# Optimization experiments

Measured on AMD Instinct MI355X. Metric: run time of the kernel, lower is better.

The kernel has to match this reference:

```python
import jax, jax.numpy as jnp
import numpy as np

# FP8 E4M3 constants (per FP8Handler)
E4M3_MAX = 240.0          # max_normal
MANTISSA_SCALE = 8.0      # 2 ** mantissa_bits (3)
SCALE_EPS = 1e-10


def setup_inputs() -> dict:
    key = jax.random.key(0)
    k1, k2, k3 = jax.random.split(key, 3)
    B, S, D_IN, D_OUT = 4, 2048, 4096, 4096
    x = jax.random.normal(k1, (B, S, D_IN), dtype=jnp.float32)
    weight = jax.random.normal(k2, (D_OUT, D_IN), dtype=jnp.float32)
    bias = jax.random.normal(k3, (D_OUT,), dtype=jnp.float32)
    return {"x": x, "weight": weight, "bias": bias}


def _fp8_e4m3_quant_dequant(w, scale):
    # FP8Handler.quantize_tensor + _simulate_e4m3_precision
    s = jnp.clip(w / scale, -E4M3_MAX, E4M3_MAX)
    s = s.astype(jnp.float16).astype(jnp.float32)  # fp16 round-trip
    q = jnp.round(s * MANTISSA_SCALE) / MANTISSA_SCALE  # mantissa truncation
    q = jnp.clip(q, -E4M3_MAX, E4M3_MAX)
    return q * scale


def reference(x, weight, bias):
    # FP8Quantizer.compute_scale: per-tensor max-abs, margin=0, fresh history
    amax = jnp.max(jnp.abs(weight))
    scale = jnp.maximum(amax / E4M3_MAX, SCALE_EPS)
    qw = _fp8_e4m3_quant_dequant(weight, scale)  # [out, in]
    # F.linear(x, qw, bias): x [b, s, in] @ qw.T [in, out] + bias
    return jnp.einsum('bsi,oi->bso', x, qw) + bias
```

## Files before the change

### kernel.cpp

```cpp
#include <hip/hip_runtime.h>
#include <hip/hip_bf16.h>
#include <hip/hip_fp16.h>

#define E4M3_MAX 240.0f

typedef __attribute__((ext_vector_type(8))) __bf16 bf16x8;
typedef __attribute__((ext_vector_type(4))) float f32x4;
typedef unsigned short ushort_t;

__device__ __forceinline__ void gload_lds16(const void* g, void* l) {
  __builtin_amdgcn_global_load_lds(
      (const __attribute__((address_space(1))) void*)g,
      (__attribute__((address_space(3))) void*)l,
      16, 0, 0);
}

__global__ void amax_abs_kernel(const float* __restrict__ w, int n4,
                                unsigned* __restrict__ amax_bits) {
  float m = 0.0f;
  const float4* w4 = (const float4*)w;
  int stride = gridDim.x * blockDim.x;
  for (int i = blockIdx.x * blockDim.x + threadIdx.x; i < n4; i += stride) {
    float4 v = w4[i];
    m = fmaxf(m, fmaxf(fmaxf(fabsf(v.x), fabsf(v.y)),
                       fmaxf(fabsf(v.z), fabsf(v.w))));
  }
  for (int off = 32; off > 0; off >>= 1)
    m = fmaxf(m, __shfl_down(m, off, 64));
  __shared__ float smax[4];
  int l = threadIdx.x & 63, wv = threadIdx.x >> 6;
  if (l == 0) smax[wv] = m;
  __syncthreads();
  if (threadIdx.x == 0) {
    float bm = fmaxf(fmaxf(smax[0], smax[1]), fmaxf(smax[2], smax[3]));
    atomicMax(amax_bits, __float_as_uint(bm));
  }
}

__global__ void quant_weight_kernel(const float* __restrict__ w,
                                    const unsigned* __restrict__ amax_bits,
                                    ushort_t* __restrict__ qw, int n4) {
  float amax = __uint_as_float(*amax_bits);
  float scale = fmaxf(amax / E4M3_MAX, 1e-10f);
  const float4* w4 = (const float4*)w;
  ushort4* q4 = (ushort4*)qw;
  int stride = gridDim.x * blockDim.x;
  for (int i = blockIdx.x * blockDim.x + threadIdx.x; i < n4; i += stride) {
    float4 v = w4[i];
    float r[4] = {v.x, v.y, v.z, v.w};
    ushort_t o[4];
#pragma unroll
    for (int j = 0; j < 4; ++j) {
      float s = fminf(fmaxf(r[j] / scale, -E4M3_MAX), E4M3_MAX);
      s = __half2float(__float2half(s));
      float q = rintf(s * 8.0f) * 0.125f;
      q = fminf(fmaxf(q, -E4M3_MAX), E4M3_MAX);
      __hip_bfloat16 h = __float2bfloat16(q * scale);
      o[j] = *(ushort_t*)&h;
    }
    ushort4 ov = {o[0], o[1], o[2], o[3]};
    q4[i] = ov;
  }
}

__global__ void cvt_bf16_kernel(const float* __restrict__ x,
                                ushort_t* __restrict__ xb, int n4) {
  const float4* x4 = (const float4*)x;
  ushort4* o4 = (ushort4*)xb;
  int stride = gridDim.x * blockDim.x;
  for (int i = blockIdx.x * blockDim.x + threadIdx.x; i < n4; i += stride) {
    float4 v = x4[i];
    __hip_bfloat16 h0 = __float2bfloat16(v.x);
    __hip_bfloat16 h1 = __float2bfloat16(v.y);
    __hip_bfloat16 h2 = __float2bfloat16(v.z);
    __hip_bfloat16 h3 = __float2bfloat16(v.w);
    ushort4 o = {*(ushort_t*)&h0, *(ushort_t*)&h1,
                 *(ushort_t*)&h2, *(ushort_t*)&h3};
    o4[i] = o;
  }
}


#define BAR() do { asm volatile("" ::: "memory"); \
                   __builtin_amdgcn_s_barrier(); \
                   asm volatile("" ::: "memory"); } while (0)
#define LGKM0() asm volatile("s_waitcnt lgkmcnt(0)" ::: "memory")
#define LGKM8() asm volatile("s_waitcnt lgkmcnt(8)" ::: "memory")
#define VMC6() asm volatile("s_waitcnt vmcnt(6)" ::: "memory")
#define VMC8() asm volatile("s_waitcnt vmcnt(8)" ::: "memory")
#define VMC0() asm volatile("s_waitcnt vmcnt(0)" ::: "memory")
#define NOVM() do {} while (0)

__global__ __launch_bounds__(512, 2) void gemm256_q(
    const ushort_t* __restrict__ A, const ushort_t* __restrict__ Bt,
    const float* __restrict__ bias, float* __restrict__ C) {
  constexpr int K = 4096, N = 4096;
  __shared__ __align__(16) ushort_t As[2][2][8192];
  __shared__ __align__(16) ushort_t Bs[2][2][8192];

  const int tid = threadIdx.x;
  const int wid = tid >> 6, lane = tid & 63;
  const int wm = wid >> 2, wn = wid & 3;
  const int lk = lane >> 4, lr = lane & 15;

  int bid = blockIdx.x;
  int swz = (bid & 7) * 64 + (bid >> 3);
  int bm = swz >> 4, bn = swz & 15;

  const ushort_t* Ab = A + (size_t)bm * 256 * K;
  const ushort_t* Bb = Bt + (size_t)bn * 256 * K;

  int offG[2];
#pragma unroll
  for (int q = 0; q < 2; ++q) {
    int s = q * 512 + tid;
    int row = s >> 3;
    int c = (s & 7) ^ (row & 7);
    offG[q] = row * K + c * 8;
  }

#define STAGE_AH(buf, kt, h)                                               \
  do { _Pragma("unroll") for (int q = 0; q < 2; ++q)                       \
    gload_lds16(Ab + (size_t)(h) * 128 * K + (kt) * 64 + offG[q],          \
                &As[buf][h][(q * 512 + wid * 64) * 8]); } while (0)
#define STAGE_BH(buf, kt, h)                                               \
  do { _Pragma("unroll") for (int q = 0; q < 2; ++q)                       \
    gload_lds16(Bb + (size_t)(h) * 128 * K + (kt) * 64 + offG[q],          \
                &Bs[buf][h][(q * 512 + wid * 64) * 8]); } while (0)

  const int abase = lr * 64;
  const int bbase = (wn & 1) * 4096 + lr * 64;
  const int bhalf = wn >> 1;
  const int xk0 = ((lk) ^ (lr & 7)) * 8;
  const int xk1 = ((4 + lk) ^ (lr & 7)) * 8;

  bf16x8 afE[4][2], afO[4][2], bfP[2][2], bfQ[2][2];
  f32x4 acc[8][4] = {};

#define RDA(AF, fi0, cb)                                                   \
  do { _Pragma("unroll") for (int i = 0; i < 4; ++i) {                     \
    AF[i][0] = *(const bf16x8*)&As[cb][wm][abase + ((fi0) + i) * 1024 + xk0]; \
    AF[i][1] = *(const bf16x8*)&As[cb][wm][abase + ((fi0) + i) * 1024 + xk1]; \
  } } while (0)
#define RDB(BF, fj0, cb)                                                   \
  do { _Pragma("unroll") for (int j = 0; j < 2; ++j) {                     \
    BF[j][0] = *(const bf16x8*)&Bs[cb][bhalf][bbase + ((fj0) + j) * 1024 + xk0]; \
    BF[j][1] = *(const bf16x8*)&Bs[cb][bhalf][bbase + ((fj0) + j) * 1024 + xk1]; \
  } } while (0)

#define MMAQ(AF, fi0, BF, fj0)                                             \
  do { __builtin_amdgcn_s_setprio(1);                                      \
    _Pragma("unroll") for (int i = 0; i < 4; ++i)                          \
      _Pragma("unroll") for (int j = 0; j < 2; ++j) {                      \
        acc[(fi0) + i][(fj0) + j] = __builtin_amdgcn_mfma_f32_16x16x32_bf16( \
            AF[i][0], BF[j][0], acc[(fi0) + i][(fj0) + j], 0, 0, 0);       \
        acc[(fi0) + i][(fj0) + j] = __builtin_amdgcn_mfma_f32_16x16x32_bf16( \
            AF[i][1], BF[j][1], acc[(fi0) + i][(fj0) + j], 0, 0, 0);       \
      }                                                                    \
    __builtin_amdgcn_s_setprio(0); } while (0)

#define BODY(u, S1, S3, S45, S78, VM4, VM8)                                \
  do {                                                                     \
                                                                  \
    RDA(afE, 0, 0); RDB(bfP, 0, 0);                                        \
    if (S1) STAGE_AH(1, (u) + 1, 1);                                       \
    LGKM8(); BAR(); LGKM0(); MMAQ(afE, 0, bfP, 0); BAR();                  \
                                                                  \
    RDB(bfQ, 2, 0);                                                        \
    BAR(); LGKM0(); MMAQ(afE, 0, bfQ, 2); BAR();                           \
                                                                  \
    RDA(afO, 4, 0);                                                        \
    if (S3) STAGE_BH(0, (u) + 2, 0);                                       \
    BAR(); LGKM0(); MMAQ(afO, 4, bfQ, 2); BAR();                           \
                                                                  \
    if (S45) { STAGE_BH(0, (u) + 2, 1); STAGE_AH(0, (u) + 2, 0); }         \
    VM4; BAR(); MMAQ(afO, 4, bfP, 0); BAR();                               \
                                                                  \
    RDA(afE, 0, 1); RDB(bfP, 0, 1);                                        \
    if (S45) STAGE_AH(0, (u) + 2, 1);                                      \
    LGKM8(); BAR(); LGKM0(); MMAQ(afE, 0, bfP, 0); BAR();                  \
                                                                  \
    RDB(bfQ, 2, 1);                                                        \
    BAR(); LGKM0(); MMAQ(afE, 0, bfQ, 2); BAR();                           \
                                                                  \
    RDA(afO, 4, 1);                                                        \
    if (S78) STAGE_BH(1, (u) + 3, 0);                                      \
    BAR(); LGKM0(); MMAQ(afO, 4, bfQ, 2); BAR();                           \
                                                                  \
    if (S78) { STAGE_BH(1, (u) + 3, 1); STAGE_AH(1, (u) + 3, 0); }         \
    VM8; BAR(); MMAQ(afO, 4, bfP, 0); BAR();                               \
  } while (0)

  STAGE_BH(0, 0, 0); STAGE_BH(0, 0, 1);
  STAGE_AH(0, 0, 0); STAGE_AH(0, 0, 1);
  STAGE_BH(1, 1, 0); STAGE_BH(1, 1, 1);
  STAGE_AH(1, 1, 0); STAGE_AH(1, 1, 1);
  VMC8();
  BAR();

  BODY(0, 0, 1, 1, 1, VMC6(), VMC6());
  for (int u = 2; u < 62; u += 2)
    BODY(u, 1, 1, 1, 1, VMC6(), VMC6());
  BODY(62, 1, 0, 0, 0, VMC0(), NOVM());

  float* Cb = C + (size_t)(bm * 256 + wm * 128) * N + bn * 256 + wn * 64;
#pragma unroll
  for (int fj = 0; fj < 4; ++fj) {
    int n = fj * 16 + lr;
    float bv = bias[bn * 256 + wn * 64 + n];
#pragma unroll
    for (int fi = 0; fi < 8; ++fi) {
      int m0 = fi * 16 + lk * 4;
#pragma unroll
      for (int r = 0; r < 4; ++r)
        Cb[(size_t)(m0 + r) * N + n] = acc[fi][fj][r] + bv;
    }
  }
}

extern "C" void kernel_launch(void* const* d_in, const int* in_sizes, int n_in,
                              void* d_out, int out_size, void* d_ws, size_t ws_size,
                              hipStream_t stream) {
  const float* x = (const float*)d_in[0];
  const float* wt = (const float*)d_in[1];
  const float* bias = (const float*)d_in[2];
  float* out = (float*)d_out;

  const int DIN = 4096;
  const int NW = in_sizes[1];
  const int M = in_sizes[0] / DIN;

  char* ws = (char*)d_ws;
  unsigned* amax_bits = (unsigned*)ws;
  ushort_t* qw = (ushort_t*)(ws + 256);
  ushort_t* xb = (ushort_t*)(ws + 256 + (size_t)NW * 2);

  hipMemsetAsync(amax_bits, 0, 4, stream);
  hipLaunchKernelGGL(amax_abs_kernel, dim3(1024), dim3(256), 0, stream,
                     wt, NW / 4, amax_bits);
  hipLaunchKernelGGL(quant_weight_kernel, dim3(2048), dim3(256), 0, stream,
                     wt, amax_bits, qw, NW / 4);
  hipLaunchKernelGGL(cvt_bf16_kernel, dim3(2048), dim3(256), 0, stream,
                     x, xb, (M * DIN) / 4);

  hipLaunchKernelGGL(gemm256_q, dim3(512), dim3(512), 0, stream,
                     xb, qw, bias, out);
}
```

Before: 351.3 us.

## Restructure GEMM main loop to prefetch next-tile fragments across tile boundary

Replaces the two-tile BODY macro with a per-tile TILE schedule. The first A and B fragments of the next K-tile are read from LDS during the current tile's later MFMA phases, using ping-pong B registers. Global-to-LDS staging for tile t+2 is issued into the just-consumed buffer, with a full vmcnt(0) wait mid-tile. This aims to hide LDS read latency at tile boundaries, at the cost of extra registers and a stricter global-load wait.

```diff
diff --git a/kernel.cpp b/kernel.cpp
--- a/kernel.cpp
+++ b/kernel.cpp
@@ -85,13 +85,10 @@
                    __builtin_amdgcn_s_barrier(); \
                    asm volatile("" ::: "memory"); } while (0)
 #define LGKM0() asm volatile("s_waitcnt lgkmcnt(0)" ::: "memory")
-#define LGKM8() asm volatile("s_waitcnt lgkmcnt(8)" ::: "memory")
-#define VMC6() asm volatile("s_waitcnt vmcnt(6)" ::: "memory")
 #define VMC8() asm volatile("s_waitcnt vmcnt(8)" ::: "memory")
 #define VMC0() asm volatile("s_waitcnt vmcnt(0)" ::: "memory")
-#define NOVM() do {} while (0)
-
-__global__ __launch_bounds__(512, 2) void gemm256_q(
+
+__global__ __launch_bounds__(512, 2) void gemm256_sb(
     const ushort_t* __restrict__ A, const ushort_t* __restrict__ Bt,
     const float* __restrict__ bias, float* __restrict__ C) {
   constexpr int K = 4096, N = 4096;
@@ -134,7 +131,7 @@
   const int xk0 = ((lk) ^ (lr & 7)) * 8;
   const int xk1 = ((4 + lk) ^ (lr & 7)) * 8;
 
-  bf16x8 afE[4][2], afO[4][2], bfP[2][2], bfQ[2][2];
+  bf16x8 afE[4][2], afO[4][2], bfQ[2][2], bfPe[2][2], bfPo[2][2];
   f32x4 acc[8][4] = {};
 
 #define RDA(AF, fi0, cb)                                                   \
@@ -159,36 +156,23 @@
       }                                                                    \
     __builtin_amdgcn_s_setprio(0); } while (0)
 
-#define BODY(u, S1, S3, S45, S78, VM4, VM8)                                \
+#define TILE(b, t, BP, BPn, DO_S, DO_R)                                    \
   do {                                                                     \
                                                                   \
-    RDA(afE, 0, 0); RDB(bfP, 0, 0);                                        \
-    if (S1) STAGE_AH(1, (u) + 1, 1);                                       \
-    LGKM8(); BAR(); LGKM0(); MMAQ(afE, 0, bfP, 0); BAR();                  \
-                                                                  \
-    RDB(bfQ, 2, 0);                                                        \
-    BAR(); LGKM0(); MMAQ(afE, 0, bfQ, 2); BAR();                           \
-                                                                  \
-    RDA(afO, 4, 0);                                                        \
-    if (S3) STAGE_BH(0, (u) + 2, 0);                                       \
+    RDB(bfQ, 2, b);                                                        \
+    BAR(); LGKM0(); MMAQ(afE, 0, BP, 0); BAR();                            \
+                                                                  \
+    RDA(afO, 4, b);                                                        \
+    BAR(); LGKM0(); MMAQ(afE, 0, bfQ, 2); VMC0(); BAR();                   \
+                                                                  \
+    if (DO_R) RDA(afE, 0, (b) ^ 1);                                        \
+    if (DO_S) STAGE_BH(b, (t) + 2, 0);                                     \
     BAR(); LGKM0(); MMAQ(afO, 4, bfQ, 2); BAR();                           \
                                                                   \
-    if (S45) { STAGE_BH(0, (u) + 2, 1); STAGE_AH(0, (u) + 2, 0); }         \
-    VM4; BAR(); MMAQ(afO, 4, bfP, 0); BAR();                               \
-                                                                  \
-    RDA(afE, 0, 1); RDB(bfP, 0, 1);                                        \
-    if (S45) STAGE_AH(0, (u) + 2, 1);                                      \
-    LGKM8(); BAR(); LGKM0(); MMAQ(afE, 0, bfP, 0); BAR();                  \
-                                                                  \
-    RDB(bfQ, 2, 1);                                                        \
-    BAR(); LGKM0(); MMAQ(afE, 0, bfQ, 2); BAR();                           \
-                                                                  \
-    RDA(afO, 4, 1);                                                        \
-    if (S78) STAGE_BH(1, (u) + 3, 0);                                      \
-    BAR(); LGKM0(); MMAQ(afO, 4, bfQ, 2); BAR();                           \
-                                                                  \
-    if (S78) { STAGE_BH(1, (u) + 3, 1); STAGE_AH(1, (u) + 3, 0); }         \
-    VM8; BAR(); MMAQ(afO, 4, bfP, 0); BAR();                               \
+    if (DO_R) RDB(BPn, 0, (b) ^ 1);                                        \
+    if (DO_S) { STAGE_BH(b, (t) + 2, 1);                                   \
+                STAGE_AH(b, (t) + 2, 0); STAGE_AH(b, (t) + 2, 1); }        \
+    BAR(); LGKM0(); MMAQ(afO, 4, BP, 0); BAR();                            \
   } while (0)
 
   STAGE_BH(0, 0, 0); STAGE_BH(0, 0, 1);
@@ -197,11 +181,14 @@
   STAGE_AH(1, 1, 0); STAGE_AH(1, 1, 1);
   VMC8();
   BAR();
-
-  BODY(0, 0, 1, 1, 1, VMC6(), VMC6());
-  for (int u = 2; u < 62; u += 2)
-    BODY(u, 1, 1, 1, 1, VMC6(), VMC6());
-  BODY(62, 1, 0, 0, 0, VMC0(), NOVM());
+  RDA(afE, 0, 0); RDB(bfPe, 0, 0);
+
+  for (int t = 0; t < 62; t += 2) {
+    TILE(0, t,     bfPe, bfPo, 1, 1);
+    TILE(1, t + 1, bfPo, bfPe, 1, 1);
+  }
+  TILE(0, 62, bfPe, bfPo, 0, 1);
+  TILE(1, 63, bfPo, bfPe, 0, 0);
 
   float* Cb = C + (size_t)(bm * 256 + wm * 128) * N + bn * 256 + wn * 64;
 #pragma unroll
@@ -243,6 +230,6 @@
   hipLaunchKernelGGL(cvt_bf16_kernel, dim3(2048), dim3(256), 0, stream,
                      x, xb, (M * DIN) / 4);
 
-  hipLaunchKernelGGL(gemm256_q, dim3(512), dim3(512), 0, stream,
+  hipLaunchKernelGGL(gemm256_sb, dim3(512), dim3(512), 0, stream,
                      xb, qw, bias, out);
 }
```

After: 445.9 us. 1.27x slower.
